# Performance work log

Hardware: AMD Instinct MI355X
Metric: run time of the kernel (lower is better)

Reference implementation:

```python
import jax, jax.numpy as jnp
import numpy as np

NEG_SLOPE = 0.2


def _segment_softmax(logits, seg, num_segments):
    m = jax.ops.segment_max(logits, seg, num_segments=num_segments)
    m = jnp.where(jnp.isfinite(m), m, 0.0)
    e = jnp.exp(logits - m[seg])
    s = jax.ops.segment_sum(e, seg, num_segments=num_segments)
    return e / (s[seg] + 1e-16)


def _gat_conv(x, src, dst, W, a_src, a_dst, b, num_nodes):
    # PyG GATConv, heads=1, concat=True, add_self_loops already applied to src/dst.
    h = x @ W                                  # [N, F_out]
    alpha_src = h @ a_src                      # [N]
    alpha_dst = h @ a_dst                      # [N]
    logits = jax.nn.leaky_relu(alpha_src[src] + alpha_dst[dst], NEG_SLOPE)  # [E]
    alpha = _segment_softmax(logits, dst, num_nodes)                        # [E]
    out = jax.ops.segment_sum(alpha[:, None] * h[src], dst, num_segments=num_nodes)
    return out + b


def setup_inputs() -> dict:
    key = jax.random.key(0)
    ks = jax.random.split(key, 16)
    N, E, F_in = 50000, 1600000, 256
    x = jax.random.normal(ks[0], (N, F_in), dtype=jnp.float32)
    edge_index = jax.random.randint(ks[1], (2, E), 0, N, dtype=jnp.int64)
    edge_attr = jax.random.normal(ks[2], (E, 1), dtype=jnp.float32)

    def glorot(k, shape):
        fan = sum(shape) if len(shape) > 1 else shape[0]
        return jax.random.normal(k, shape, dtype=jnp.float32) * jnp.sqrt(2.0 / fan)

    params = {
        "W1": glorot(ks[3], (F_in, 48)), "as1": glorot(ks[4], (48,)),
        "ad1": glorot(ks[5], (48,)),     "b1": jnp.zeros((48,), jnp.float32),
        "W2": glorot(ks[6], (48, 60)),   "as2": glorot(ks[7], (60,)),
        "ad2": glorot(ks[8], (60,)),     "b2": jnp.zeros((60,), jnp.float32),
        "W3": glorot(ks[9], (60, 1)),    "as3": glorot(ks[10], (1,)),
        "ad3": glorot(ks[11], (1,)),     "b3": jnp.zeros((1,), jnp.float32),
    }
    return {"x": x, "edge_index": edge_index, "edge_attr": edge_attr, **params}


def reference(x, edge_index, edge_attr, W1, as1, ad1, b1, W2, as2, ad2, b2, W3, as3, ad3, b3):
    # edge_attr is accepted but ignored: GATConv was built without edge_dim, so no lin_edge.
    N = x.shape[0]
    loops = jnp.arange(N, dtype=edge_index.dtype)
    src = jnp.concatenate([edge_index[0], loops])  # add_self_loops=True
    dst = jnp.concatenate([edge_index[1], loops])
    h = jax.nn.relu(_gat_conv(x, src, dst, W1, as1, ad1, b1, N))
    h = jax.nn.relu(_gat_conv(h, src, dst, W2, as2, ad2, b2, N))
    h = _gat_conv(h, src, dst, W3, as3, ad3, b3, N)
    return h.reshape(-1)  # flatten -> [N]
```

## Files before the change

### kernel.cpp

```cpp
#include <hip/hip_runtime.h>
#include <cstdint>
#include <cstddef>


__device__ __forceinline__ float leaky(float v) { return v > 0.f ? v : 0.2f * v; }

__device__ __forceinline__ unsigned short f2bf(float x) {
    unsigned int u = __float_as_uint(x);
    u = (u + 0x7FFFu + ((u >> 16) & 1u)) >> 16;
    return (unsigned short)u;
}
__device__ __forceinline__ float bf2f(unsigned short b) {
    return __uint_as_float(((unsigned int)b) << 16);
}

#define BSHIFT 7
#define BCAP   5120
#define CTILE  8192


__global__ __launch_bounds__(256) void coarse_bin_kernel(
    const int* __restrict__ ei, unsigned int* __restrict__ staged,
    int* __restrict__ gcursor, int E, int K) {
    __shared__ int hist[512];
    __shared__ int rank[512];
    __shared__ int base[512];
    for (int b = threadIdx.x; b < K; b += 256) { hist[b] = 0; rank[b] = 0; }
    __syncthreads();

    int e0 = blockIdx.x * CTILE;
    int e1 = min(E, e0 + CTILE);

    for (int e = e0 + threadIdx.x; e < e1; e += 256) {
        int d = ei[E + e];
        atomicAdd(&hist[d >> BSHIFT], 1);
    }
    __syncthreads();

    for (int b = threadIdx.x; b < K; b += 256) {
        int c = hist[b];
        base[b] = c ? atomicAdd(&gcursor[b], c) : 0;
    }
    __syncthreads();

    for (int e = e0 + threadIdx.x; e < e1; e += 256) {
        int s = ei[e];
        int d = ei[E + e];
        int b = d >> BSHIFT;
        int r = atomicAdd(&rank[b], 1);
        staged[(size_t)b * BCAP + base[b] + r] =
            ((unsigned int)(d & ((1 << BSHIFT) - 1)) << 16) | (unsigned int)s;
    }
}


__global__ __launch_bounds__(512) void bucket_scan_kernel(
    const int* __restrict__ gcursor, int* __restrict__ bbase, int K) {
    __shared__ int sh[512];
    int t = threadIdx.x;
    int v = (t < K) ? gcursor[t] : 0;
    sh[t] = v;
    __syncthreads();
    for (int off = 1; off < 512; off <<= 1) {
        int a = (t >= off) ? sh[t - off] : 0;
        __syncthreads();
        sh[t] += a;
        __syncthreads();
    }
    if (t < K) bbase[t] = sh[t] - v;
}


__global__ __launch_bounds__(256) void fine_sort_kernel(
    const unsigned int* __restrict__ staged, const int* __restrict__ gcursor,
    const int* __restrict__ bbase, int* __restrict__ rowptr, int* __restrict__ csr,
    int N, int E) {
    __shared__ int cnt[128];
    __shared__ int off[128];
    __shared__ int lcsr[BCAP];
    const int b = blockIdx.x;
    const int t = threadIdx.x;
    const int c = gcursor[b];
    const int gb = bbase[b];
    const unsigned int* rec = staged + (size_t)b * BCAP;

    if (t < 128) cnt[t] = 0;
    __syncthreads();

    for (int i = t; i < c; i += 256) atomicAdd(&cnt[rec[i] >> 16], 1);
    __syncthreads();

    if (t < 128) off[t] = cnt[t];
    __syncthreads();
    for (int s = 1; s < 128; s <<= 1) {
        int a = (t >= s && t < 128) ? off[t - s] : 0;
        __syncthreads();
        if (t < 128) off[t] += a;
        __syncthreads();
    }

    if (t < 128) {
        int excl = off[t] - cnt[t];
        int n = (b << BSHIFT) + t;
        if (n <= N) rowptr[n] = gb + excl;
        cnt[t] = excl;
    }
    if (b == 0 && t == 0) rowptr[N] = E;
    __syncthreads();

    for (int i = t; i < c; i += 256) {
        unsigned int r = rec[i];
        int p = atomicAdd(&cnt[r >> 16], 1);
        lcsr[p] = (int)(r & 0xFFFFu);
    }
    __syncthreads();

    for (int i = t; i < c; i += 256) csr[gb + i] = lcsr[i];
}


template <int FIN, int FOUT, int FT>
__global__ __launch_bounds__(256) void gemm_sgpr_kernel(
    const float* __restrict__ X, const float* __restrict__ W,
    const float* __restrict__ avs, const float* __restrict__ avd,
    unsigned short* __restrict__ hb, float* __restrict__ asrc, float* __restrict__ adst,
    int N) {
    static_assert(4 * FT == FOUT, "FT must be FOUT/4");
    __shared__ float red[2][4][64];

    const int wid  = __builtin_amdgcn_readfirstlane(threadIdx.x >> 6);
    const int lane = threadIdx.x & 63;
    const int n    = blockIdx.x * 64 + lane;
    const int nc   = (n < N) ? n : N - 1;
    const int fbase = wid * FT;

    const float* xrow = X + (size_t)nc * FIN;

    float acc[FT];
#pragma unroll
    for (int c = 0; c < FT; c++) acc[c] = 0.f;

#pragma unroll
    for (int k = 0; k < FIN; k += 4) {
        float4 xv = *(const float4*)(xrow + k);
        const float* w0 = W + (size_t)k * FOUT + fbase;
#pragma unroll
        for (int c = 0; c < FT; c++) {
            acc[c] = fmaf(xv.x, w0[c],            acc[c]);
            acc[c] = fmaf(xv.y, w0[FOUT + c],     acc[c]);
            acc[c] = fmaf(xv.z, w0[2 * FOUT + c], acc[c]);
            acc[c] = fmaf(xv.w, w0[3 * FOUT + c], acc[c]);
        }
    }

    float ps = 0.f, pd = 0.f;
#pragma unroll
    for (int c = 0; c < FT; c++) {
        ps = fmaf(acc[c], avs[fbase + c], ps);
        pd = fmaf(acc[c], avd[fbase + c], pd);
    }
    red[0][wid][lane] = ps;
    red[1][wid][lane] = pd;

    if (n < N) {
        if constexpr ((FT & 1) == 0) {
            unsigned int* dst = (unsigned int*)(hb + (size_t)n * 64 + fbase);
#pragma unroll
            for (int c = 0; c < FT; c += 2) {
                unsigned int pk = (unsigned int)f2bf(acc[c]) |
                                  ((unsigned int)f2bf(acc[c + 1]) << 16);
                dst[c >> 1] = pk;
            }
        } else {
#pragma unroll
            for (int c = 0; c < FT; c++)
                hb[(size_t)n * 64 + fbase + c] = f2bf(acc[c]);
        }
    }

    __syncthreads();
    if (threadIdx.x < 64 && n < N) {
        float s = red[0][0][lane] + red[0][1][lane] + red[0][2][lane] + red[0][3][lane];
        float d = red[1][0][lane] + red[1][1][lane] + red[1][2][lane] + red[1][3][lane];
        asrc[n] = s;
        adst[n] = d;
    }
}


#define CHUNK 128

template <int FOUT, bool RELU>
__global__ __launch_bounds__(256) void agg_bf16_kernel(
    const int* __restrict__ rowptr, const int* __restrict__ csr,
    const float* __restrict__ asrc, const float* __restrict__ adst,
    const unsigned short* __restrict__ hb, const float* __restrict__ bias,
    float* __restrict__ OUT, int N) {
    __shared__ int2 wslds[4][CHUNK];
    const int wv = threadIdx.x >> 6;
    int n = blockIdx.x * 4 + wv;
    if (n >= N) return;
    const int lane = threadIdx.x & 63;
    const int rs = rowptr[n], re = rowptr[n + 1];
    const float ad_n = adst[n];
    const float wself = __expf(leaky(asrc[n] + ad_n));
    const int fc = (lane < FOUT) ? lane : FOUT - 1;

    float acc = wself * bf2f(hb[(size_t)n * 64 + fc]);
    float wpart = 0.f;

    for (int base = rs; base < re; base += CHUNK) {
        const int cnt = min(CHUNK, re - base);
        if (lane < cnt) {
            int s = csr[base + lane];
            float w = __expf(leaky(asrc[s] + ad_n));
            wpart += w;
            wslds[wv][lane] = make_int2(s, __float_as_int(w));
        }
        int i = 0;
        for (; i + 8 <= cnt; i += 8) {
            int2 p[8];
#pragma unroll
            for (int u = 0; u < 8; u++) p[u] = wslds[wv][i + u];
            float hv[8];
#pragma unroll
            for (int u = 0; u < 8; u++) hv[u] = bf2f(hb[(size_t)p[u].x * 64 + fc]);
#pragma unroll
            for (int u = 0; u < 8; u++) acc = fmaf(__int_as_float(p[u].y), hv[u], acc);
        }
        for (; i < cnt; i++) {
            int2 pp = wslds[wv][i];
            acc = fmaf(__int_as_float(pp.y), bf2f(hb[(size_t)pp.x * 64 + fc]), acc);
        }
    }

#pragma unroll
    for (int off = 32; off; off >>= 1) wpart += __shfl_xor(wpart, off, 64);
    float ssum = wpart + wself;

    if (lane < FOUT) {
        float o = acc / (ssum + 1e-16f) + bias[lane];
        if (RELU) o = fmaxf(o, 0.f);
        OUT[(size_t)n * FOUT + lane] = o;
    }
}


__global__ __launch_bounds__(256) void agg_bf16_h3_kernel(
    const int* __restrict__ rowptr, const int* __restrict__ csr,
    const float* __restrict__ asrc, const float* __restrict__ adst,
    const unsigned short* __restrict__ hb, const float* __restrict__ bias,
    const float* __restrict__ W3, float* __restrict__ h3, int N) {
    constexpr int FOUT = 60;
    __shared__ int2 wslds[4][CHUNK];
    const int wv = threadIdx.x >> 6;
    int n = blockIdx.x * 4 + wv;
    if (n >= N) return;
    const int lane = threadIdx.x & 63;
    const int rs = rowptr[n], re = rowptr[n + 1];
    const float ad_n = adst[n];
    const float wself = __expf(leaky(asrc[n] + ad_n));
    const int fc = (lane < FOUT) ? lane : FOUT - 1;

    float acc = wself * bf2f(hb[(size_t)n * 64 + fc]);
    float wpart = 0.f;

    for (int base = rs; base < re; base += CHUNK) {
        const int cnt = min(CHUNK, re - base);
        if (lane < cnt) {
            int s = csr[base + lane];
            float w = __expf(leaky(asrc[s] + ad_n));
            wpart += w;
            wslds[wv][lane] = make_int2(s, __float_as_int(w));
        }
        int i = 0;
        for (; i + 8 <= cnt; i += 8) {
            int2 p[8];
#pragma unroll
            for (int u = 0; u < 8; u++) p[u] = wslds[wv][i + u];
            float hv[8];
#pragma unroll
            for (int u = 0; u < 8; u++) hv[u] = bf2f(hb[(size_t)p[u].x * 64 + fc]);
#pragma unroll
            for (int u = 0; u < 8; u++) acc = fmaf(__int_as_float(p[u].y), hv[u], acc);
        }
        for (; i < cnt; i++) {
            int2 pp = wslds[wv][i];
            acc = fmaf(__int_as_float(pp.y), bf2f(hb[(size_t)pp.x * 64 + fc]), acc);
        }
    }

#pragma unroll
    for (int off = 32; off; off >>= 1) wpart += __shfl_xor(wpart, off, 64);
    float ssum = wpart + wself;

    float t = 0.f;
    if (lane < FOUT) {
        float o = fmaxf(acc / (ssum + 1e-16f) + bias[lane], 0.f);
        t = o * W3[lane];
    }
#pragma unroll
    for (int off = 32; off; off >>= 1) t += __shfl_xor(t, off, 64);
    if (lane == 0) h3[n] = t;
}


__global__ __launch_bounds__(256) void agg1_kernel(
    const int* __restrict__ rowptr, const int* __restrict__ csr,
    const float* __restrict__ h3,
    const float* __restrict__ as3p, const float* __restrict__ ad3p,
    const float* __restrict__ bias, float* __restrict__ OUT, int N) {
    int n = blockIdx.x * 4 + (threadIdx.x >> 6);
    if (n >= N) return;
    int lane = threadIdx.x & 63;
    int rs = rowptr[n], re = rowptr[n + 1];
    const float a_s = as3p[0];
    float hn = h3[n];
    float adn = ad3p[0] * hn;
    float wself = __expf(leaky(a_s * hn + adn));

    float ssum = 0.f, accv = 0.f;
    for (int e = rs + lane; e < re; e += 64) {
        float hs = h3[csr[e]];
        float w = __expf(leaky(a_s * hs + adn));
        ssum += w;
        accv = fmaf(w, hs, accv);
    }
#pragma unroll
    for (int off = 32; off; off >>= 1) {
        ssum += __shfl_xor(ssum, off, 64);
        accv += __shfl_xor(accv, off, 64);
    }
    ssum += wself;
    accv = fmaf(wself, hn, accv);
    if (lane == 0) OUT[n] = accv / (ssum + 1e-16f) + bias[0];
}


extern "C" void kernel_launch(void* const* d_in, const int* in_sizes, int n_in,
                              void* d_out, int out_size, void* d_ws, size_t ws_size,
                              hipStream_t stream) {
    const float* x      = (const float*)d_in[0];
    const int*   ei     = (const int*)d_in[1];
    const float* W1  = (const float*)d_in[3];
    const float* as1 = (const float*)d_in[4];
    const float* ad1 = (const float*)d_in[5];
    const float* b1  = (const float*)d_in[6];
    const float* W2  = (const float*)d_in[7];
    const float* as2 = (const float*)d_in[8];
    const float* ad2 = (const float*)d_in[9];
    const float* b2  = (const float*)d_in[10];
    const float* W3  = (const float*)d_in[11];
    const float* as3 = (const float*)d_in[12];
    const float* ad3 = (const float*)d_in[13];
    const float* b3  = (const float*)d_in[14];

    const int N = in_sizes[0] / 256;
    const int E = in_sizes[1] / 2;
    const int K = (N + (1 << BSHIFT) - 1) >> BSHIFT;

    char* p = (char*)d_ws;
    auto alloc = [&](size_t bytes) -> void* {
        void* r = (void*)p;
        p += ((bytes + 255) / 256) * 256;
        return r;
    };
    int*   gcursor = (int*)alloc(512 * 4);
    int*   bbase   = (int*)alloc(512 * 4);
    int*   rowptr  = (int*)alloc(((size_t)N + 1) * 4);
    int*   csr     = (int*)alloc((size_t)E * 4);
    unsigned short* hb = (unsigned short*)alloc((size_t)N * 64 * 2);
    float* actbuf  = (float*)alloc((size_t)N * 48 * 4);
    float* h3      = (float*)alloc((size_t)N * 4);
    float* asrc    = (float*)alloc((size_t)N * 4);
    float* adst    = (float*)alloc((size_t)N * 4);
    unsigned int* staged = (unsigned int*)actbuf;

    hipMemsetAsync(gcursor, 0, 512 * 4, stream);
    int cblocks = (E + CTILE - 1) / CTILE;
    coarse_bin_kernel<<<cblocks, 256, 0, stream>>>(ei, staged, gcursor, E, K);
    bucket_scan_kernel<<<1, 512, 0, stream>>>(gcursor, bbase, K);
    fine_sort_kernel<<<K, 256, 0, stream>>>(staged, gcursor, bbase, rowptr, csr, N, E);

    int gblocks = (N + 63) / 64;
    int ablocks = (N + 3) / 4;

    gemm_sgpr_kernel<256, 48, 12><<<gblocks, 256, 0, stream>>>(
        x, W1, as1, ad1, hb, asrc, adst, N);
    agg_bf16_kernel<48, true><<<ablocks, 256, 0, stream>>>(rowptr, csr, asrc, adst, hb, b1, actbuf, N);

    gemm_sgpr_kernel<48, 60, 15><<<gblocks, 256, 0, stream>>>(
        actbuf, W2, as2, ad2, hb, asrc, adst, N);
    agg_bf16_h3_kernel<<<ablocks, 256, 0, stream>>>(rowptr, csr, asrc, adst, hb, b2, W3, h3, N);

    agg1_kernel<<<ablocks, 256, 0, stream>>>(rowptr, csr, h3, as3, ad3, b3, (float*)d_out, N);
}
```

Baseline: 297.8 us.

## Split first-layer GEMM over K across waves with LDS reduction

Replaces the first-layer GEMM, which split output columns across the four waves, with a kernel that splits the input dimension: each wave computes all 48 outputs for a quarter of K, with contiguous float4 loads of x. The partial sums are reduced through padded shared memory, and the attention dot products and bf16 packing are then done by four threads per node. The goal is to read each x row once with wide loads instead of having every wave re-read it. The cost is 48 accumulators per thread, which raises register pressure, plus an LDS reduction and a block barrier.

```diff
diff --git a/kernel.cpp b/kernel.cpp
--- a/kernel.cpp
+++ b/kernel.cpp
@@ -116,6 +116,79 @@
     __syncthreads();
 
     for (int i = t; i < c; i += 256) csr[gb + i] = lcsr[i];
+}
+
+
+template <int FIN, int FOUT>
+__global__ __launch_bounds__(256) void gemm_ksplit_kernel(
+    const float* __restrict__ X, const float* __restrict__ W,
+    const float* __restrict__ avs, const float* __restrict__ avd,
+    unsigned short* __restrict__ hb, float* __restrict__ asrc, float* __restrict__ adst,
+    int N) {
+    static_assert(FIN % 16 == 0, "FIN multiple of 16");
+    static_assert(FOUT % 8 == 0, "FOUT multiple of 8 (b128 + dword bf16 packs)");
+    constexpr int K4  = FIN / 4;
+    constexpr int CPT = FOUT / 4;
+    constexpr int PAD = 52;
+    __shared__ float red[4][64][PAD];
+
+    const int wid  = __builtin_amdgcn_readfirstlane(threadIdx.x >> 6);
+    const int lane = threadIdx.x & 63;
+    const int n    = blockIdx.x * 64 + lane;
+    const int nc   = (n < N) ? n : N - 1;
+    const float* xrow  = X + (size_t)nc * FIN + wid * K4;
+    const float* wbase = W + (size_t)wid * K4 * FOUT;
+
+    float acc[FOUT];
+#pragma unroll
+    for (int c = 0; c < FOUT; c++) acc[c] = 0.f;
+
+#pragma unroll
+    for (int k = 0; k < K4; k += 4) {
+        float4 xv = *(const float4*)(xrow + k);
+        const float* w0 = wbase + (size_t)k * FOUT;
+#pragma unroll
+        for (int c = 0; c < FOUT; c++) {
+            acc[c] = fmaf(xv.x, w0[c],            acc[c]);
+            acc[c] = fmaf(xv.y, w0[FOUT + c],     acc[c]);
+            acc[c] = fmaf(xv.z, w0[2 * FOUT + c], acc[c]);
+            acc[c] = fmaf(xv.w, w0[3 * FOUT + c], acc[c]);
+        }
+    }
+
+#pragma unroll
+    for (int c = 0; c < FOUT; c += 4)
+        *(float4*)&red[wid][lane][c] = make_float4(acc[c], acc[c + 1], acc[c + 2], acc[c + 3]);
+    __syncthreads();
+
+    {
+        const int node = threadIdx.x >> 2;
+        const int cg   = (threadIdx.x & 3) * CPT;
+        const int gn   = blockIdx.x * 64 + node;
+        float h[CPT];
+#pragma unroll
+        for (int c = 0; c < CPT; c++)
+            h[c] = red[0][node][cg + c] + red[1][node][cg + c] +
+                   red[2][node][cg + c] + red[3][node][cg + c];
+
+        float ps = 0.f, pd = 0.f;
+#pragma unroll
+        for (int c = 0; c < CPT; c++) {
+            ps = fmaf(h[c], avs[cg + c], ps);
+            pd = fmaf(h[c], avd[cg + c], pd);
+        }
+        ps += __shfl_xor(ps, 1, 64); pd += __shfl_xor(pd, 1, 64);
+        ps += __shfl_xor(ps, 2, 64); pd += __shfl_xor(pd, 2, 64);
+
+        if (gn < N) {
+            if ((threadIdx.x & 3) == 0) { asrc[gn] = ps; adst[gn] = pd; }
+            unsigned int* dst = (unsigned int*)(hb + (size_t)gn * 64 + cg);
+#pragma unroll
+            for (int c = 0; c < CPT; c += 2)
+                dst[c >> 1] = (unsigned int)f2bf(h[c]) |
+                              ((unsigned int)f2bf(h[c + 1]) << 16);
+        }
+    }
 }
 
 
@@ -385,7 +458,7 @@
     int gblocks = (N + 63) / 64;
     int ablocks = (N + 3) / 4;
 
-    gemm_sgpr_kernel<256, 48, 12><<<gblocks, 256, 0, stream>>>(
+    gemm_ksplit_kernel<256, 48><<<gblocks, 256, 0, stream>>>(
         x, W1, as1, ad1, hb, asrc, adst, N);
     agg_bf16_kernel<48, true><<<ablocks, 256, 0, stream>>>(rowptr, csr, asrc, adst, hb, b1, actbuf, N);
 
```

New measurement: 298.2 us. About the same (+0.1%).
